# Kernel tuning notes

Measured on AMD Instinct MI355X. Metric: run time of the kernel, lower is better.

The kernel has to match this reference:

```python
import jax, jax.numpy as jnp
import numpy as np

D_MODEL = 1024
NUM_HEADS = 16
D_K = D_MODEL // NUM_HEADS


def setup_inputs() -> dict:
    key = jax.random.key(0)
    ks = jax.random.split(key, 8)
    B, S = 2, 2048
    s = 1.0 / np.sqrt(D_MODEL)
    return {
        "query": jax.random.normal(ks[0], (B, S, D_MODEL), jnp.float32),
        "key": jax.random.normal(ks[1], (B, S, D_MODEL), jnp.float32),
        "value": jax.random.normal(ks[2], (B, S, D_MODEL), jnp.float32),
        "Wq": jax.random.normal(ks[3], (D_MODEL, D_MODEL), jnp.float32) * s,
        "bq": jnp.zeros((D_MODEL,), jnp.float32),
        "Wk": jax.random.normal(ks[4], (D_MODEL, D_MODEL), jnp.float32) * s,
        "bk": jnp.zeros((D_MODEL,), jnp.float32),
        "Wv": jax.random.normal(ks[5], (D_MODEL, D_K), jnp.float32) * s,
        "bv": jnp.zeros((D_K,), jnp.float32),
        "Wo": jax.random.normal(ks[6], (D_K, D_MODEL), jnp.float32) * (1.0 / np.sqrt(D_K)),
        "bo": jnp.zeros((D_MODEL,), jnp.float32),
    }


def reference(query, key, value, Wq, bq, Wk, bk, Wv, bv, Wo, bo):
    B, S, _ = query.shape
    scale = jnp.sqrt(jnp.asarray(D_K, query.dtype))
    # Per-head Q, K: [B, H, S, d_k]
    Q = (query @ Wq + bq).reshape(B, S, NUM_HEADS, D_K).transpose(0, 2, 1, 3)
    K = (key @ Wk + bk).reshape(B, -1, NUM_HEADS, D_K).transpose(0, 2, 1, 3)
    # Shared V across heads: [B, S, d_k]
    V = value @ Wv + bv
    scores = jnp.einsum("bhqd,bhkd->bhqk", Q, K) / scale
    attn = jax.nn.softmax(scores, axis=-1)
    avg_attn = attn.mean(axis=1)            # [B, S, S] head-averaged weights
    attn_output = jnp.einsum("bqk,bkd->bqd", avg_attn, V)
    output = attn_output @ Wo + bo
    return (output, avg_attn)
```

## Files before the change

### kernel.cpp

```cpp
#include <hip/hip_runtime.h>

#define BATCH 2
#define SEQ   2048
#define DMODEL 1024
#define NHEAD 16
#define DK    64
#define MROWS (BATCH * SEQ)
#define KSPLIT 4

using bf16x8 = __attribute__((ext_vector_type(8))) short;
using f32x4  = __attribute__((ext_vector_type(4))) float;

__device__ __forceinline__ unsigned short f2bf_rne(float x) {
    unsigned u = __float_as_uint(x);
    u += 0x7FFFu + ((u >> 16) & 1u);
    return (unsigned short)(u >> 16);
}
__device__ __forceinline__ float bf2f(unsigned short h) {
    return __uint_as_float((unsigned)h << 16);
}

__device__ __forceinline__ long long qf_addr(int row, int d) {
    const int qt = row >> 4, lid = row & 15;
    const int hh = d >> 6, ch = (d >> 3) & 7, j = d & 7;
    return ((((long long)qt * NHEAD + hh) * 8 + ch) * 16 + lid) * 8 + j;
}

__global__ __launch_bounds__(256) void conv_split_kernel(
    const float* __restrict__ x, unsigned short* __restrict__ hi,
    unsigned short* __restrict__ lo)
{
    const long long i = ((long long)blockIdx.x * 256 + threadIdx.x) * 4;
    float4 v = *(const float4*)&x[i];
    ushort4 h4, l4;
    unsigned short h;
    h = f2bf_rne(v.x); h4.x = h; l4.x = f2bf_rne(v.x - bf2f(h));
    h = f2bf_rne(v.y); h4.y = h; l4.y = f2bf_rne(v.y - bf2f(h));
    h = f2bf_rne(v.z); h4.z = h; l4.z = f2bf_rne(v.z - bf2f(h));
    h = f2bf_rne(v.w); h4.w = h; l4.w = f2bf_rne(v.w - bf2f(h));
    *(ushort4*)&hi[i] = h4;
    *(ushort4*)&lo[i] = l4;
}

__global__ __launch_bounds__(256) void conv_splitT_kernel(
    const float* __restrict__ W, unsigned short* __restrict__ hiT,
    unsigned short* __restrict__ loT)
{
    const int k0 = blockIdx.y * 64;
    const int n0 = blockIdx.x * 64;
    const int tid = threadIdx.x;
    __shared__ float T[64][68];
#pragma unroll
    for (int it = 0; it < 4; ++it) {
        const int r = it * 16 + (tid >> 4);
        const int c = (tid & 15) * 4;
        float4 v = *(const float4*)&W[(long long)(k0 + r) * DMODEL + n0 + c];
        T[r][c] = v.x; T[r][c + 1] = v.y; T[r][c + 2] = v.z; T[r][c + 3] = v.w;
    }
    __syncthreads();
#pragma unroll
    for (int it = 0; it < 4; ++it) {
        const int n = it * 16 + (tid >> 4);
        const int kc = (tid & 15) * 4;
        ushort4 h4, l4;
        float v; unsigned short h;
        v = T[kc + 0][n]; h = f2bf_rne(v); h4.x = h; l4.x = f2bf_rne(v - bf2f(h));
        v = T[kc + 1][n]; h = f2bf_rne(v); h4.y = h; l4.y = f2bf_rne(v - bf2f(h));
        v = T[kc + 2][n]; h = f2bf_rne(v); h4.z = h; l4.z = f2bf_rne(v - bf2f(h));
        v = T[kc + 3][n]; h = f2bf_rne(v); h4.w = h; l4.w = f2bf_rne(v - bf2f(h));
        const long long off = (long long)(n0 + n) * DMODEL + k0 + kc;
        *(ushort4*)&hiT[off] = h4;
        *(ushort4*)&loT[off] = l4;
    }
}

#define PROW 40

__global__ __launch_bounds__(256) void proj_mfma_kernel(
    const unsigned short* __restrict__ AH, const unsigned short* __restrict__ AL,
    const unsigned short* __restrict__ BTH, const unsigned short* __restrict__ BTL,
    const float* __restrict__ bias,
    unsigned short* __restrict__ OH, unsigned short* __restrict__ OL, int fragQ)
{
    const int n0 = blockIdx.x * 128;
    const int m0 = blockIdx.y * 128;
    const int tid = threadIdx.x;
    const int w = tid >> 6, lane = tid & 63;
    const int wm = w >> 1, wn = w & 1;
    const int quad = lane >> 4, lid = lane & 15;

    __shared__ unsigned short As[2][128][PROW];
    __shared__ unsigned short Bs[2][128][PROW];

    f32x4 acc[4][4] = {};

    for (int k0 = 0; k0 < DMODEL; k0 += 32) {
        __syncthreads();
#pragma unroll
        for (int it = 0; it < 4; ++it) {
            const int cell = it * 256 + tid;
            const int half = cell >> 9;
            const int row  = (cell >> 2) & 127;
            const int c    = cell & 3;
            const unsigned short* a = half ? AL : AH;
            uint4 v = *(const uint4*)&a[(long long)(m0 + row) * DMODEL + k0 + c * 8];
            *(uint4*)&As[half][row][c * 8] = v;
            const unsigned short* b = half ? BTL : BTH;
            uint4 u = *(const uint4*)&b[(long long)(n0 + row) * DMODEL + k0 + c * 8];
            *(uint4*)&Bs[half][row][c * 8] = u;
        }
        __syncthreads();

        bf16x8 af[2][4], bf_[2][4];
#pragma unroll
        for (int mt = 0; mt < 4; ++mt) {
            const int r = wm * 64 + mt * 16 + lid;
            af[0][mt] = *(const bf16x8*)&As[0][r][quad * 8];
            af[1][mt] = *(const bf16x8*)&As[1][r][quad * 8];
        }
#pragma unroll
        for (int nt = 0; nt < 4; ++nt) {
            const int r = wn * 64 + nt * 16 + lid;
            bf_[0][nt] = *(const bf16x8*)&Bs[0][r][quad * 8];
            bf_[1][nt] = *(const bf16x8*)&Bs[1][r][quad * 8];
        }
#pragma unroll
        for (int mt = 0; mt < 4; ++mt)
#pragma unroll
            for (int nt = 0; nt < 4; ++nt) {
                acc[mt][nt] = __builtin_amdgcn_mfma_f32_16x16x32_bf16(af[0][mt], bf_[0][nt], acc[mt][nt], 0, 0, 0);
                acc[mt][nt] = __builtin_amdgcn_mfma_f32_16x16x32_bf16(af[0][mt], bf_[1][nt], acc[mt][nt], 0, 0, 0);
                acc[mt][nt] = __builtin_amdgcn_mfma_f32_16x16x32_bf16(af[1][mt], bf_[0][nt], acc[mt][nt], 0, 0, 0);
            }
    }

    float bv[4];
#pragma unroll
    for (int nt = 0; nt < 4; ++nt)
        bv[nt] = bias[n0 + wn * 64 + nt * 16 + lid];

#pragma unroll
    for (int mt = 0; mt < 4; ++mt)
#pragma unroll
        for (int nt = 0; nt < 4; ++nt) {
            const int col = n0 + wn * 64 + nt * 16 + lid;
#pragma unroll
            for (int r = 0; r < 4; ++r) {
                const int row = m0 + wm * 64 + mt * 16 + quad * 4 + r;
                const float val = acc[mt][nt][r] + bv[nt];
                const unsigned short h = f2bf_rne(val);
                const unsigned short l = f2bf_rne(val - bf2f(h));
                if (fragQ) {
                    const long long fa = qf_addr(row, col);
                    OH[fa] = h; OL[fa] = l;
                } else {
                    const long long off = (long long)row * DMODEL + col;
                    OH[off] = h; OL[off] = l;
                }
            }
        }
}

__global__ __launch_bounds__(256) void gemm_bias_kernel(
    const float* __restrict__ A, long long sA,
    const float* __restrict__ W, long long sW,
    const float* __restrict__ bias,
    float* __restrict__ C, long long sC,
    int M, int N, int K)
{
    A += (long long)blockIdx.z * sA;
    W += (long long)blockIdx.z * sW;
    C += (long long)blockIdx.z * sC;
    const int n0 = blockIdx.x * 64;
    const int m0 = blockIdx.y * 64;

    __shared__ float As[16][68];
    __shared__ float Bs[16][68];

    const int tid = threadIdx.x;
    const int tm = (tid >> 4) << 2;
    const int tn = (tid & 15) << 2;
    const int arow = tid >> 2, ak = (tid & 3) << 2;
    const int brow = tid >> 4, bn = (tid & 15) << 2;

    float acc[4][4] = {};

    for (int k0 = 0; k0 < K; k0 += 16) {
        float4 av = *(const float4*)&A[(long long)(m0 + arow) * K + k0 + ak];
        float4 wv = *(const float4*)&W[(long long)(k0 + brow) * N + n0 + bn];
        As[ak + 0][arow] = av.x;
        As[ak + 1][arow] = av.y;
        As[ak + 2][arow] = av.z;
        As[ak + 3][arow] = av.w;
        *(float4*)&Bs[brow][bn] = wv;
        __syncthreads();
#pragma unroll
        for (int kk = 0; kk < 16; ++kk) {
            float4 a4 = *(const float4*)&As[kk][tm];
            float4 b4 = *(const float4*)&Bs[kk][tn];
            float aa[4] = {a4.x, a4.y, a4.z, a4.w};
            float bb[4] = {b4.x, b4.y, b4.z, b4.w};
#pragma unroll
            for (int i = 0; i < 4; ++i)
#pragma unroll
                for (int j = 0; j < 4; ++j)
                    acc[i][j] = fmaf(aa[i], bb[j], acc[i][j]);
        }
        __syncthreads();
    }

    float4 bv = make_float4(0.f, 0.f, 0.f, 0.f);
    if (bias) bv = *(const float4*)&bias[n0 + tn];
#pragma unroll
    for (int i = 0; i < 4; ++i) {
        float4 o = make_float4(acc[i][0] + bv.x, acc[i][1] + bv.y,
                               acc[i][2] + bv.z, acc[i][3] + bv.w);
        *(float4*)&C[(long long)(m0 + tm + i) * N + n0 + tn] = o;
    }
}

__global__ __launch_bounds__(256) void gemm_splitk_kernel(
    const float* __restrict__ A, long long sA,
    const float* __restrict__ W, long long sW,
    float* __restrict__ P,
    int M, int N, int K, int nsplit)
{
    const int nbatch = gridDim.z / nsplit;
    const int b = blockIdx.z / nsplit;
    const int s = blockIdx.z % nsplit;
    A += (long long)b * sA;
    W += (long long)b * sW;
    float* Pout = P + ((long long)s * nbatch + b) * M * N;

    const int n0 = blockIdx.x * 64;
    const int m0 = blockIdx.y * 64;
    const int kb = s * (K / nsplit);
    const int kl = K / nsplit;

    __shared__ float As[16][68];
    __shared__ float Bs[16][68];

    const int tid = threadIdx.x;
    const int tm = (tid >> 4) << 2;
    const int tn = (tid & 15) << 2;
    const int arow = tid >> 2, ak = (tid & 3) << 2;
    const int brow = tid >> 4, bn = (tid & 15) << 2;

    float acc[4][4] = {};

    for (int k0 = 0; k0 < kl; k0 += 16) {
        float4 av = *(const float4*)&A[(long long)(m0 + arow) * K + kb + k0 + ak];
        float4 wv = *(const float4*)&W[(long long)(kb + k0 + brow) * N + n0 + bn];
        As[ak + 0][arow] = av.x;
        As[ak + 1][arow] = av.y;
        As[ak + 2][arow] = av.z;
        As[ak + 3][arow] = av.w;
        *(float4*)&Bs[brow][bn] = wv;
        __syncthreads();
#pragma unroll
        for (int kk = 0; kk < 16; ++kk) {
            float4 a4 = *(const float4*)&As[kk][tm];
            float4 b4 = *(const float4*)&Bs[kk][tn];
            float aa[4] = {a4.x, a4.y, a4.z, a4.w};
            float bb[4] = {b4.x, b4.y, b4.z, b4.w};
#pragma unroll
            for (int i = 0; i < 4; ++i)
#pragma unroll
                for (int j = 0; j < 4; ++j)
                    acc[i][j] = fmaf(aa[i], bb[j], acc[i][j]);
        }
        __syncthreads();
    }

#pragma unroll
    for (int i = 0; i < 4; ++i) {
        float4 o = make_float4(acc[i][0], acc[i][1], acc[i][2], acc[i][3]);
        *(float4*)&Pout[(long long)(m0 + tm + i) * N + n0 + tn] = o;
    }
}

__global__ __launch_bounds__(256) void reduce_bias_kernel(
    const float* __restrict__ P, const float* __restrict__ bias,
    float* __restrict__ C, long long stride, int nsplit, int N)
{
    const long long i = ((long long)blockIdx.x * 256 + threadIdx.x) * 4;
    float4 s = *(const float4*)&P[i];
    for (int k = 1; k < nsplit; ++k) {
        float4 v = *(const float4*)&P[(long long)k * stride + i];
        s.x += v.x; s.y += v.y; s.z += v.z; s.w += v.w;
    }
    if (bias) {
        const int n = (int)(i % N);
        float4 b4 = *(const float4*)&bias[n];
        s.x += b4.x; s.y += b4.y; s.z += b4.z; s.w += b4.w;
    }
    *(float4*)&C[i] = s;
}

#define HALF_USH 8192
#define TILE_USH 16384

__device__ __forceinline__ void stage_issue(
    const unsigned short* __restrict__ Khi, const unsigned short* __restrict__ Klo,
    unsigned short* KsBuf, long long grow0, int h, int w, int lane)
{
    const int rsub = lane >> 3;
    const int slot = (lane & 7) ^ rsub;
#pragma unroll
    for (int it = 0; it < 4; ++it) {
        const int c = it * 8 + w;
        const int half = c >> 4;
        const int row  = (c & 15) * 8 + rsub;
        const unsigned short* src = half ? Klo : Khi;
        const unsigned short* g = &src[(grow0 + row) * DMODEL + h * 64 + slot * 8];
        __builtin_amdgcn_global_load_lds(
            (const __attribute__((address_space(1))) unsigned int*)g,
            (__attribute__((address_space(3))) unsigned int*)(KsBuf + c * 512),
            16, 0, 0);
    }
}

__device__ __forceinline__ f32x4 mfma3(bf16x8 ah, bf16x8 al, bf16x8 bh, bf16x8 bl, f32x4 s) {
    s = __builtin_amdgcn_mfma_f32_16x16x32_bf16(ah, bh, s, 0, 0, 0);
    s = __builtin_amdgcn_mfma_f32_16x16x32_bf16(ah, bl, s, 0, 0, 0);
    s = __builtin_amdgcn_mfma_f32_16x16x32_bf16(al, bh, s, 0, 0, 0);
    return s;
}

__global__ __launch_bounds__(512, 4) void attn_stats_kernel(
    const unsigned short* __restrict__ QfH, const unsigned short* __restrict__ QfL,
    const unsigned short* __restrict__ Khi, const unsigned short* __restrict__ Klo,
    float* __restrict__ lsum)
{
    const int q0 = blockIdx.x * 256;
    const int h  = blockIdx.y;
    const int b  = blockIdx.z >> 2;
    const int kbase = (blockIdx.z & 3) * (SEQ / KSPLIT);
    const int tid = threadIdx.x;
    const int w = tid >> 6, lane = tid & 63;
    const int quad = lane >> 4, lid = lane & 15;

    __shared__ unsigned short Ks[2 * TILE_USH];

    bf16x8 ah[2][2], al[2][2];
#pragma unroll
    for (int mt = 0; mt < 2; ++mt) {
        const long long qt = (long long)(b * SEQ + q0) / 16 + w * 2 + mt;
#pragma unroll
        for (int ks = 0; ks < 2; ++ks) {
            const long long fa = (((qt * NHEAD + h) * 8 + (quad + 4 * ks)) * 16 + lid) * 8;
            ah[mt][ks] = *(const bf16x8*)&QfH[fa];
            al[mt][ks] = *(const bf16x8*)&QfL[fa];
        }
    }

    float ls[2][4] = {};
    const long long grow0 = (long long)b * SEQ + kbase;

    stage_issue(Khi, Klo, Ks, grow0, h, w, lane);
    __syncthreads();

    for (int kc = 0; kc < SEQ / KSPLIT; kc += 128) {
        const int buf = (kc >> 7) & 1;
        if (kc + 128 < SEQ / KSPLIT)
            stage_issue(Khi, Klo, Ks + (buf ^ 1) * TILE_USH,
                        grow0 + kc + 128, h, w, lane);
        const unsigned short* Kc = Ks + buf * TILE_USH;

#pragma unroll
        for (int kt = 0; kt < 8; ++kt) {
            const int rr = kt * 16 + lid;
            const int sw = rr & 7;
            bf16x8 bh[2], bl[2];
#pragma unroll
            for (int ks = 0; ks < 2; ++ks) {
                const int o = rr * 64 + (((quad + 4 * ks) ^ sw) * 8);
                bh[ks] = *(const bf16x8*)&Kc[o];
                bl[ks] = *(const bf16x8*)&Kc[HALF_USH + o];
            }
#pragma unroll
            for (int mt = 0; mt < 2; ++mt) {
                f32x4 s = {0.f, 0.f, 0.f, 0.f};
#pragma unroll
                for (int ks = 0; ks < 2; ++ks)
                    s = mfma3(ah[mt][ks], al[mt][ks], bh[ks], bl[ks], s);
#pragma unroll
                for (int r = 0; r < 4; ++r)
                    ls[mt][r] += __expf(s[r] * 0.125f);
            }
        }
        __syncthreads();
    }

#pragma unroll
    for (int off = 1; off < 16; off <<= 1)
#pragma unroll
        for (int mt = 0; mt < 2; ++mt)
#pragma unroll
            for (int r = 0; r < 4; ++r)
                ls[mt][r] += __shfl_xor(ls[mt][r], off);

    if (lid == 0) {
        const long long base = ((long long)(b * NHEAD + h)) * SEQ + q0 + w * 32 + quad * 4;
#pragma unroll
        for (int mt = 0; mt < 2; ++mt)
#pragma unroll
            for (int r = 0; r < 4; ++r)
                atomicAdd(&lsum[base + mt * 16 + r], ls[mt][r]);
    }
}

__global__ __launch_bounds__(256) void recip_kernel(float* __restrict__ p) {
    const int i = blockIdx.x * 256 + threadIdx.x;
    p[i] = 0.0625f / p[i];
}

__global__ __launch_bounds__(512, 4) void attn_avg_kernel(
    const unsigned short* __restrict__ QfH, const unsigned short* __restrict__ QfL,
    const unsigned short* __restrict__ Khi, const unsigned short* __restrict__ Klo,
    const float* __restrict__ cIn, float* __restrict__ avg)
{
    const int q0 = blockIdx.x * 128;
    const int k0 = blockIdx.y * 128;
    const int b  = blockIdx.z;
    const int tid = threadIdx.x;
    const int w = tid >> 6, lane = tid & 63;
    const int wq = w >> 1, wk = w & 1;
    const int quad = lane >> 4, lid = lane & 15;

    __shared__ unsigned short Ks[2 * TILE_USH];

    f32x4 acc[2][4] = {};
    const long long grow0 = (long long)b * SEQ + k0;

    stage_issue(Khi, Klo, Ks, grow0, 0, w, lane);
    __syncthreads();

    for (int h = 0; h < NHEAD; ++h) {
        bf16x8 ah[2][2], al[2][2];
        float c_[2][4];
#pragma unroll
        for (int mt = 0; mt < 2; ++mt) {
            const long long qt = (long long)(b * SEQ + q0) / 16 + wq * 2 + mt;
#pragma unroll
            for (int ks = 0; ks < 2; ++ks) {
                const long long fa = (((qt * NHEAD + h) * 8 + (quad + 4 * ks)) * 16 + lid) * 8;
                ah[mt][ks] = *(const bf16x8*)&QfH[fa];
                al[mt][ks] = *(const bf16x8*)&QfL[fa];
            }
            const long long cb = ((long long)(b * NHEAD + h)) * SEQ + q0 + wq * 32 + mt * 16 + quad * 4;
#pragma unroll
            for (int r = 0; r < 4; ++r)
                c_[mt][r] = cIn[cb + r];
        }

        const int buf = h & 1;
        if (h + 1 < NHEAD)
            stage_issue(Khi, Klo, Ks + (buf ^ 1) * TILE_USH,
                        grow0, h + 1, w, lane);
        const unsigned short* Kc = Ks + buf * TILE_USH;

#pragma unroll
        for (int kt = 0; kt < 4; ++kt) {
            const int rr = wk * 64 + kt * 16 + lid;
            const int sw = rr & 7;
            bf16x8 bh[2], bl[2];
#pragma unroll
            for (int ks = 0; ks < 2; ++ks) {
                const int o = rr * 64 + (((quad + 4 * ks) ^ sw) * 8);
                bh[ks] = *(const bf16x8*)&Kc[o];
                bl[ks] = *(const bf16x8*)&Kc[HALF_USH + o];
            }
#pragma unroll
            for (int mt = 0; mt < 2; ++mt) {
                f32x4 s = {0.f, 0.f, 0.f, 0.f};
#pragma unroll
                for (int ks = 0; ks < 2; ++ks)
                    s = mfma3(ah[mt][ks], al[mt][ks], bh[ks], bl[ks], s);
#pragma unroll
                for (int r = 0; r < 4; ++r)
                    acc[mt][kt][r] = fmaf(__expf(s[r] * 0.125f), c_[mt][r], acc[mt][kt][r]);
            }
        }
        __syncthreads();
    }

#pragma unroll
    for (int mt = 0; mt < 2; ++mt)
#pragma unroll
        for (int kt = 0; kt < 4; ++kt)
#pragma unroll
            for (int r = 0; r < 4; ++r) {
                const int q = q0 + wq * 32 + mt * 16 + quad * 4 + r;
                avg[((long long)(b * SEQ + q)) * SEQ + k0 + wk * 64 + kt * 16 + lid] = acc[mt][kt][r];
            }
}

extern "C" void kernel_launch(void* const* d_in, const int* in_sizes, int n_in,
                              void* d_out, int out_size, void* d_ws, size_t ws_size,
                              hipStream_t stream)
{
    const float* query = (const float*)d_in[0];
    const float* key   = (const float*)d_in[1];
    const float* value = (const float*)d_in[2];
    const float* Wq    = (const float*)d_in[3];
    const float* bq    = (const float*)d_in[4];
    const float* Wk    = (const float*)d_in[5];
    const float* bk    = (const float*)d_in[6];
    const float* Wv    = (const float*)d_in[7];
    const float* bv    = (const float*)d_in[8];
    const float* Wo    = (const float*)d_in[9];
    const float* bo    = (const float*)d_in[10];

    float* out = (float*)d_out;
    float* avg = out + (long long)BATCH * SEQ * DMODEL;

    const long long QKN = (long long)MROWS * DMODEL;
    unsigned short* QfH = (unsigned short*)d_ws;
    unsigned short* QfL = QfH + QKN;
    unsigned short* Khi = QfL + QKN;
    unsigned short* Klo = Khi + QKN;
    unsigned short* AspH = Klo + QKN;
    unsigned short* AspL = AspH + QKN;
    unsigned short* WTh  = AspL + QKN;
    unsigned short* WTl  = WTh + (long long)DMODEL * DMODEL;
    float* Vb   = (float*)(WTl + (long long)DMODEL * DMODEL);
    float* lBuf = Vb + (long long)MROWS * DK;
    float* ao   = lBuf + (long long)BATCH * NHEAD * SEQ;

    float* Pv  = (float*)AspH;
    float* Pav = (float*)QfH;

    dim3 blk(256);
    hipMemsetAsync(lBuf, 0, (size_t)BATCH * NHEAD * SEQ * sizeof(float), stream);

    const int convGrid = (int)(QKN / (256 * 4));
    dim3 tGrid(DMODEL / 64, DMODEL / 64);
    dim3 pGrid(DMODEL / 128, MROWS / 128);

    conv_split_kernel<<<convGrid, blk, 0, stream>>>(query, AspH, AspL);
    conv_splitT_kernel<<<tGrid, blk, 0, stream>>>(Wq, WTh, WTl);
    proj_mfma_kernel<<<pGrid, blk, 0, stream>>>(AspH, AspL, WTh, WTl, bq, QfH, QfL, 1);

    conv_split_kernel<<<convGrid, blk, 0, stream>>>(key, AspH, AspL);
    conv_splitT_kernel<<<tGrid, blk, 0, stream>>>(Wk, WTh, WTl);
    proj_mfma_kernel<<<pGrid, blk, 0, stream>>>(AspH, AspL, WTh, WTl, bk, Khi, Klo, 0);

    gemm_splitk_kernel<<<dim3(DK / 64, MROWS / 64, 16), blk, 0, stream>>>(
        value, 0, Wv, 0, Pv, MROWS, DK, DMODEL, 16);
    reduce_bias_kernel<<<dim3((int)((long long)MROWS * DK / 1024)), blk, 0, stream>>>(
        Pv, bv, Vb, (long long)MROWS * DK, 16, DK);

    attn_stats_kernel<<<dim3(SEQ / 256, NHEAD, BATCH * KSPLIT), dim3(512), 0, stream>>>(
        QfH, QfL, Khi, Klo, lBuf);
    recip_kernel<<<dim3(BATCH * NHEAD * SEQ / 256), blk, 0, stream>>>(lBuf);

    attn_avg_kernel<<<dim3(SEQ / 128, SEQ / 128, BATCH), dim3(512), 0, stream>>>(
        QfH, QfL, Khi, Klo, lBuf, avg);

    gemm_splitk_kernel<<<dim3(DK / 64, SEQ / 64, BATCH * 32), blk, 0, stream>>>(
        avg, (long long)SEQ * SEQ, Vb, (long long)SEQ * DK, Pav, SEQ, DK, SEQ, 32);
    reduce_bias_kernel<<<dim3((int)((long long)MROWS * DK / 1024)), blk, 0, stream>>>(
        Pav, nullptr, ao, (long long)MROWS * DK, 32, DK);

    gemm_bias_kernel<<<dim3(DMODEL / 64, MROWS / 64, 1), blk, 0, stream>>>(
        ao, 0, Wo, 0, bo, out, 0, MROWS, DMODEL, DK);
}
```

Baseline: 411.1 us.

## Retile projection GEMM with direct global-to-LDS loads; remap attn_avg waves

The projection GEMM switches to a 128x64 output tile with a 64-wide K step. Its operands are loaded with global_load_lds straight into an XOR-swizzled LDS layout instead of through registers into padded rows, and it now declares launch bounds allowing 2 blocks per SU. The grid doubles in the N direction. In attn_avg, each wave now covers 16 query rows across all 128 keys instead of a 32x64 sub-tile. This halves the Q fragment loads per wave but reads each K fragment by every wave, so LDS traffic rises.

```diff
diff --git a/kernel.cpp b/kernel.cpp
--- a/kernel.cpp
+++ b/kernel.cpp
@@ -74,79 +74,99 @@
     }
 }
 
-#define PROW 40
-
-__global__ __launch_bounds__(256) void proj_mfma_kernel(
+#define PA_HALF 8192
+#define PA_TILE 16384
+#define PB_HALF 4096
+#define PB_TILE 8192
+
+__global__ __launch_bounds__(256, 2) void proj_mfma_kernel(
     const unsigned short* __restrict__ AH, const unsigned short* __restrict__ AL,
     const unsigned short* __restrict__ BTH, const unsigned short* __restrict__ BTL,
     const float* __restrict__ bias,
     unsigned short* __restrict__ OH, unsigned short* __restrict__ OL, int fragQ)
 {
-    const int n0 = blockIdx.x * 128;
+    const int n0 = blockIdx.x * 64;
     const int m0 = blockIdx.y * 128;
     const int tid = threadIdx.x;
     const int w = tid >> 6, lane = tid & 63;
-    const int wm = w >> 1, wn = w & 1;
     const int quad = lane >> 4, lid = lane & 15;
-
-    __shared__ unsigned short As[2][128][PROW];
-    __shared__ unsigned short Bs[2][128][PROW];
-
-    f32x4 acc[4][4] = {};
-
-    for (int k0 = 0; k0 < DMODEL; k0 += 32) {
-        __syncthreads();
+    const int rsub = lane >> 3;
+    const int slot = (lane & 7) ^ rsub;
+
+    __shared__ unsigned short As[PA_TILE];
+    __shared__ unsigned short Bs[PB_TILE];
+
+    f32x4 acc[2][4] = {};
+
+    for (int kc = 0; kc < DMODEL; kc += 64) {
+        __syncthreads();
+#pragma unroll
+        for (int it = 0; it < 8; ++it) {
+            const int c = it * 4 + w;
+            const int half = c >> 4;
+            const int row  = (c & 15) * 8 + rsub;
+            const unsigned short* src = half ? AL : AH;
+            const unsigned short* g = &src[(long long)(m0 + row) * DMODEL + kc + slot * 8];
+            __builtin_amdgcn_global_load_lds(
+                (const __attribute__((address_space(1))) unsigned int*)g,
+                (__attribute__((address_space(3))) unsigned int*)(As + c * 512),
+                16, 0, 0);
+        }
 #pragma unroll
         for (int it = 0; it < 4; ++it) {
-            const int cell = it * 256 + tid;
-            const int half = cell >> 9;
-            const int row  = (cell >> 2) & 127;
-            const int c    = cell & 3;
-            const unsigned short* a = half ? AL : AH;
-            uint4 v = *(const uint4*)&a[(long long)(m0 + row) * DMODEL + k0 + c * 8];
-            *(uint4*)&As[half][row][c * 8] = v;
-            const unsigned short* b = half ? BTL : BTH;
-            uint4 u = *(const uint4*)&b[(long long)(n0 + row) * DMODEL + k0 + c * 8];
-            *(uint4*)&Bs[half][row][c * 8] = u;
-        }
-        __syncthreads();
-
-        bf16x8 af[2][4], bf_[2][4];
-#pragma unroll
-        for (int mt = 0; mt < 4; ++mt) {
-            const int r = wm * 64 + mt * 16 + lid;
-            af[0][mt] = *(const bf16x8*)&As[0][r][quad * 8];
-            af[1][mt] = *(const bf16x8*)&As[1][r][quad * 8];
-        }
+            const int c = it * 4 + w;
+            const int half = c >> 3;
+            const int row  = (c & 7) * 8 + rsub;
+            const unsigned short* src = half ? BTL : BTH;
+            const unsigned short* g = &src[(long long)(n0 + row) * DMODEL + kc + slot * 8];
+            __builtin_amdgcn_global_load_lds(
+                (const __attribute__((address_space(1))) unsigned int*)g,
+                (__attribute__((address_space(3))) unsigned int*)(Bs + c * 512),
+                16, 0, 0);
+        }
+        __syncthreads();
+
+#pragma unroll
+        for (int ks = 0; ks < 2; ++ks) {
+            bf16x8 ah[2], al_[2], bh[4], bl[4];
+#pragma unroll
+            for (int mt = 0; mt < 2; ++mt) {
+                const int r = w * 32 + mt * 16 + lid;
+                const int o = r * 64 + (((quad + 4 * ks) ^ (r & 7)) * 8);
+                ah[mt]  = *(const bf16x8*)&As[o];
+                al_[mt] = *(const bf16x8*)&As[PA_HALF + o];
+            }
+#pragma unroll
+            for (int nt = 0; nt < 4; ++nt) {
+                const int rn = nt * 16 + lid;
+                const int o = rn * 64 + (((quad + 4 * ks) ^ (rn & 7)) * 8);
+                bh[nt] = *(const bf16x8*)&Bs[o];
+                bl[nt] = *(const bf16x8*)&Bs[PB_HALF + o];
+            }
+#pragma unroll
+            for (int mt = 0; mt < 2; ++mt)
+#pragma unroll
+                for (int nt = 0; nt < 4; ++nt) {
+                    acc[mt][nt] = __builtin_amdgcn_mfma_f32_16x16x32_bf16(ah[mt],  bh[nt], acc[mt][nt], 0, 0, 0);
+                    acc[mt][nt] = __builtin_amdgcn_mfma_f32_16x16x32_bf16(ah[mt],  bl[nt], acc[mt][nt], 0, 0, 0);
+                    acc[mt][nt] = __builtin_amdgcn_mfma_f32_16x16x32_bf16(al_[mt], bh[nt], acc[mt][nt], 0, 0, 0);
+                }
+        }
+    }
+
+    float bv[4];
+#pragma unroll
+    for (int nt = 0; nt < 4; ++nt)
+        bv[nt] = bias[n0 + nt * 16 + lid];
+
+#pragma unroll
+    for (int mt = 0; mt < 2; ++mt)
 #pragma unroll
         for (int nt = 0; nt < 4; ++nt) {
-            const int r = wn * 64 + nt * 16 + lid;
-            bf_[0][nt] = *(const bf16x8*)&Bs[0][r][quad * 8];
-            bf_[1][nt] = *(const bf16x8*)&Bs[1][r][quad * 8];
-        }
-#pragma unroll
-        for (int mt = 0; mt < 4; ++mt)
-#pragma unroll
-            for (int nt = 0; nt < 4; ++nt) {
-                acc[mt][nt] = __builtin_amdgcn_mfma_f32_16x16x32_bf16(af[0][mt], bf_[0][nt], acc[mt][nt], 0, 0, 0);
-                acc[mt][nt] = __builtin_amdgcn_mfma_f32_16x16x32_bf16(af[0][mt], bf_[1][nt], acc[mt][nt], 0, 0, 0);
-                acc[mt][nt] = __builtin_amdgcn_mfma_f32_16x16x32_bf16(af[1][mt], bf_[0][nt], acc[mt][nt], 0, 0, 0);
-            }
-    }
-
-    float bv[4];
-#pragma unroll
-    for (int nt = 0; nt < 4; ++nt)
-        bv[nt] = bias[n0 + wn * 64 + nt * 16 + lid];
-
-#pragma unroll
-    for (int mt = 0; mt < 4; ++mt)
-#pragma unroll
-        for (int nt = 0; nt < 4; ++nt) {
-            const int col = n0 + wn * 64 + nt * 16 + lid;
+            const int col = n0 + nt * 16 + lid;
 #pragma unroll
             for (int r = 0; r < 4; ++r) {
-                const int row = m0 + wm * 64 + mt * 16 + quad * 4 + r;
+                const int row = m0 + w * 32 + mt * 16 + quad * 4 + r;
                 const float val = acc[mt][nt][r] + bv[nt];
                 const unsigned short h = f2bf_rne(val);
                 const unsigned short l = f2bf_rne(val - bf2f(h));
@@ -425,34 +445,30 @@
     const int b  = blockIdx.z;
     const int tid = threadIdx.x;
     const int w = tid >> 6, lane = tid & 63;
-    const int wq = w >> 1, wk = w & 1;
     const int quad = lane >> 4, lid = lane & 15;
 
     __shared__ unsigned short Ks[2 * TILE_USH];
 
-    f32x4 acc[2][4] = {};
+    f32x4 acc[8] = {};
     const long long grow0 = (long long)b * SEQ + k0;
+    const long long qt = (long long)(b * SEQ + q0) / 16 + w;
 
     stage_issue(Khi, Klo, Ks, grow0, 0, w, lane);
     __syncthreads();
 
     for (int h = 0; h < NHEAD; ++h) {
-        bf16x8 ah[2][2], al[2][2];
-        float c_[2][4];
-#pragma unroll
-        for (int mt = 0; mt < 2; ++mt) {
-            const long long qt = (long long)(b * SEQ + q0) / 16 + wq * 2 + mt;
-#pragma unroll
-            for (int ks = 0; ks < 2; ++ks) {
-                const long long fa = (((qt * NHEAD + h) * 8 + (quad + 4 * ks)) * 16 + lid) * 8;
-                ah[mt][ks] = *(const bf16x8*)&QfH[fa];
-                al[mt][ks] = *(const bf16x8*)&QfL[fa];
-            }
-            const long long cb = ((long long)(b * NHEAD + h)) * SEQ + q0 + wq * 32 + mt * 16 + quad * 4;
-#pragma unroll
-            for (int r = 0; r < 4; ++r)
-                c_[mt][r] = cIn[cb + r];
-        }
+        bf16x8 ah[2], al[2];
+        float c_[4];
+#pragma unroll
+        for (int ks = 0; ks < 2; ++ks) {
+            const long long fa = (((qt * NHEAD + h) * 8 + (quad + 4 * ks)) * 16 + lid) * 8;
+            ah[ks] = *(const bf16x8*)&QfH[fa];
+            al[ks] = *(const bf16x8*)&QfL[fa];
+        }
+        const long long cb = ((long long)(b * NHEAD + h)) * SEQ + q0 + w * 16 + quad * 4;
+#pragma unroll
+        for (int r = 0; r < 4; ++r)
+            c_[r] = cIn[cb + r];
 
         const int buf = h & 1;
         if (h + 1 < NHEAD)
@@ -461,8 +477,8 @@
         const unsigned short* Kc = Ks + buf * TILE_USH;
 
 #pragma unroll
-        for (int kt = 0; kt < 4; ++kt) {
-            const int rr = wk * 64 + kt * 16 + lid;
+        for (int kt = 0; kt < 8; ++kt) {
+            const int rr = kt * 16 + lid;
             const int sw = rr & 7;
             bf16x8 bh[2], bl[2];
 #pragma unroll
@@ -471,29 +487,24 @@
                 bh[ks] = *(const bf16x8*)&Kc[o];
                 bl[ks] = *(const bf16x8*)&Kc[HALF_USH + o];
             }
-#pragma unroll
-            for (int mt = 0; mt < 2; ++mt) {
-                f32x4 s = {0.f, 0.f, 0.f, 0.f};
-#pragma unroll
-                for (int ks = 0; ks < 2; ++ks)
-                    s = mfma3(ah[mt][ks], al[mt][ks], bh[ks], bl[ks], s);
-#pragma unroll
-                for (int r = 0; r < 4; ++r)
-                    acc[mt][kt][r] = fmaf(__expf(s[r] * 0.125f), c_[mt][r], acc[mt][kt][r]);
-            }
-        }
-        __syncthreads();
-    }
-
-#pragma unroll
-    for (int mt = 0; mt < 2; ++mt)
-#pragma unroll
-        for (int kt = 0; kt < 4; ++kt)
-#pragma unroll
-            for (int r = 0; r < 4; ++r) {
-                const int q = q0 + wq * 32 + mt * 16 + quad * 4 + r;
-                avg[((long long)(b * SEQ + q)) * SEQ + k0 + wk * 64 + kt * 16 + lid] = acc[mt][kt][r];
-            }
+            f32x4 s = {0.f, 0.f, 0.f, 0.f};
+#pragma unroll
+            for (int ks = 0; ks < 2; ++ks)
+                s = mfma3(ah[ks], al[ks], bh[ks], bl[ks], s);
+#pragma unroll
+            for (int r = 0; r < 4; ++r)
+                acc[kt][r] = fmaf(__expf(s[r] * 0.125f), c_[r], acc[kt][r]);
+        }
+        __syncthreads();
+    }
+
+#pragma unroll
+    for (int kt = 0; kt < 8; ++kt)
+#pragma unroll
+        for (int r = 0; r < 4; ++r) {
+            const int q = q0 + w * 16 + quad * 4 + r;
+            avg[((long long)(b * SEQ + q)) * SEQ + k0 + kt * 16 + lid] = acc[kt][r];
+        }
 }
 
 extern "C" void kernel_launch(void* const* d_in, const int* in_sizes, int n_in,
@@ -536,7 +547,7 @@
 
     const int convGrid = (int)(QKN / (256 * 4));
     dim3 tGrid(DMODEL / 64, DMODEL / 64);
-    dim3 pGrid(DMODEL / 128, MROWS / 128);
+    dim3 pGrid(DMODEL / 64, MROWS / 128);
 
     conv_split_kernel<<<convGrid, blk, 0, stream>>>(query, AspH, AspL);
     conv_splitT_kernel<<<tGrid, blk, 0, stream>>>(Wq, WTh, WTl);
```

Result: faster. 359.1 us (-12.7%).
